# Kernel optimization log

Measured on AMD Instinct MI355X. Metric: run time of the kernel, lower is better.

The kernel has to match this reference:

```python
import jax, jax.numpy as jnp
import numpy as np
from jax import lax

MAX_LEN = 50
MAX_STATES = 50
STATE_DIM = MAX_STATES + 3  # 53
LSTM = 32
EMB = 8
VOCAB = 20
N_NODES = 131072
N_EDGES = 65536
B = 4096
NODES_PER_GRAPH = 32
ACTION_SIZE = 53


def setup_inputs() -> dict:
    key = jax.random.key(0)
    ks = jax.random.split(key, 32)
    x = jax.random.normal(ks[0], (N_NODES, 55), jnp.float32)
    src_num = jax.random.uniform(ks[1], (N_EDGES, STATE_DIM), jnp.float32)
    tgt_num = jax.random.uniform(ks[2], (N_EDGES, STATE_DIM), jnp.float32)
    regex_tokens = jax.random.randint(ks[3], (N_EDGES, MAX_LEN), 0, VOCAB)
    edge_index = jax.random.randint(ks[4], (2, N_EDGES), 0, N_NODES)
    batch = jnp.repeat(jnp.arange(B, dtype=jnp.int32), NODES_PER_GRAPH)
    # frozen embedding (padding_idx=0 -> row 0 zero) + frozen bidirectional LSTM params
    emb = (jax.random.normal(ks[5], (VOCAB, EMB)) * 0.1).at[0].set(0.0)
    def lp(k1, k2, k3):
        return (jax.random.normal(k1, (4 * LSTM, EMB)) * 0.1,
                jax.random.normal(k2, (4 * LSTM, LSTM)) * 0.1,
                jax.random.normal(k3, (4 * LSTM,)) * 0.1)  # b = b_ih + b_hh combined
    w_ih_f, w_hh_f, b_f = lp(ks[6], ks[7], ks[8])
    w_ih_b, w_hh_b, b_b = lp(ks[9], ks[10], ks[11])
    def lin(k, din, dout):
        kw, kb = jax.random.split(k)
        return (jax.random.normal(kw, (din, dout)) * 0.05,
                jax.random.normal(kb, (dout,)) * 0.05)
    p1_w, p1_b = lin(ks[12], 289, 128)
    p2_w, p2_b = lin(ks[13], 128, 64)
    p3_w, p3_b = lin(ks[14], 64, 32)
    p4_w, p4_b = lin(ks[15], 32, 1)
    v1_w, v1_b = lin(ks[16], 289, 32)
    v2_w, v2_b = lin(ks[17], 32, 1)
    return dict(x=x, src_num=src_num, tgt_num=tgt_num, regex_tokens=regex_tokens,
                edge_index=edge_index, batch=batch, emb=emb,
                w_ih_f=w_ih_f, w_hh_f=w_hh_f, b_f=b_f,
                w_ih_b=w_ih_b, w_hh_b=w_hh_b, b_b=b_b,
                p1_w=p1_w, p1_b=p1_b, p2_w=p2_w, p2_b=p2_b,
                p3_w=p3_w, p3_b=p3_b, p4_w=p4_w, p4_b=p4_b,
                v1_w=v1_w, v1_b=v1_b, v2_w=v2_w, v2_b=v2_b,
                num_graphs=B, action_size=ACTION_SIZE)


def _lstm_mean(xs, w_ih, w_hh, b):
    # xs: [T, E, in]; returns mean over time of hidden states, [E, H]
    T, E, _ = xs.shape
    H = w_hh.shape[1]
    def step(carry, xt):
        h, c, acc = carry
        z = xt @ w_ih.T + h @ w_hh.T + b  # [E, 4H], torch gate order i,f,g,o
        i, f, g, o = jnp.split(z, 4, axis=-1)
        c = jax.nn.sigmoid(f) * c + jax.nn.sigmoid(i) * jnp.tanh(g)
        h = jax.nn.sigmoid(o) * jnp.tanh(c)
        return (h, c, acc + h), None
    z0 = jnp.zeros((E, H), xs.dtype)
    (h, c, acc), _ = lax.scan(step, (z0, z0, z0), xs)
    return acc / T


def _mean_pool(feats, idx, num):
    s = jax.ops.segment_sum(feats, idx, num_segments=num)
    cnt = jax.ops.segment_sum(jnp.ones((feats.shape[0], 1), feats.dtype), idx, num_segments=num)
    return s / jnp.maximum(cnt, 1.0)


def reference(x, src_num, tgt_num, regex_tokens, edge_index, batch, emb,
              w_ih_f, w_hh_f, b_f, w_ih_b, w_hh_b, b_b,
              p1_w, p1_b, p2_w, p2_b, p3_w, p3_b, p4_w, p4_b,
              v1_w, v1_b, v2_w, v2_b, num_graphs, action_size):
    # frozen EmbeddingWithLSTM: embed -> bidirectional LSTM -> mean over time
    xs = emb[regex_tokens].transpose(1, 0, 2)  # [T, E, EMB]
    mean_f = _lstm_mean(xs, w_ih_f, w_hh_f, b_f)
    mean_b = _lstm_mean(xs[::-1], w_ih_b, w_hh_b, b_b)  # mean of reversed == mean
    regex_feat = jnp.concatenate([mean_f, mean_b], axis=-1)  # [E, 64]

    src, tgt = edge_index[0], edge_index[1]
    n = x.shape[0]
    out_tr = _mean_pool(jnp.concatenate([tgt_num, regex_feat], -1), src, n)
    in_tr = _mean_pool(jnp.concatenate([src_num, regex_feat], -1), tgt, n)
    xc = jnp.concatenate([x, in_tr, out_tr], axis=-1)  # [N, 289]

    s = _mean_pool(xc, batch, num_graphs)  # [B, 289]
    v = jax.nn.relu(s @ v1_w + v1_b) @ v2_w + v2_b  # [B, 1]

    pi = jax.nn.relu(xc @ p1_w + p1_b)
    pi = jax.nn.relu(pi @ p2_w + p2_b)
    pi = jax.nn.relu(pi @ p3_w + p3_b)
    pi = pi @ p4_w + p4_b  # [N, 1]

    # vectorized ragged pack: per-graph running index (batch is sorted/contiguous)
    counts = jax.ops.segment_sum(jnp.ones_like(batch), batch, num_segments=num_graphs)
    offsets = jnp.concatenate([jnp.zeros((1,), counts.dtype), jnp.cumsum(counts)[:-1]])
    pos = jnp.arange(batch.shape[0], dtype=counts.dtype) - offsets[batch]
    new_x = jnp.full((num_graphs, action_size), -999.0, xc.dtype).at[batch, pos].set(pi[:, 0])
    return jax.nn.log_softmax(new_x, axis=1), v
```

## Files before the change

### kernel.cpp

```cpp
#include <hip/hip_runtime.h>
#include <hip/hip_bf16.h>
#include <cstdint>
#include <cstddef>

typedef __hip_bfloat16 bf16;
typedef __attribute__((ext_vector_type(8))) short short8;
typedef __attribute__((ext_vector_type(4))) float f32x4;
typedef __attribute__((ext_vector_type(4))) int i32x4;

#define NE 65536
#define NN 131072
#define TLEN 50
#define NB 4096
#define ACT 53
#define FEATF 120
#define NSLOT 12

static constexpr size_t OFF_FEAT_IN  = 0;
static constexpr size_t OFF_FEAT_OUT = OFF_FEAT_IN + (size_t)NE * FEATF;
static constexpr size_t OFF_CNT_IN   = OFF_FEAT_OUT + (size_t)NE * FEATF;
static constexpr size_t OFF_CNT_OUT  = OFF_CNT_IN + NN;
static constexpr size_t OFF_SLOT_IN  = OFF_CNT_OUT + NN;
static constexpr size_t OFF_SLOT_OUT = OFF_SLOT_IN + (size_t)NN * NSLOT;
static constexpr size_t OFF_ZXF      = OFF_SLOT_OUT + (size_t)NN * NSLOT;
static constexpr size_t OFF_WFRAG    = OFF_ZXF + 4096;
static constexpr size_t OFF_B1       = OFF_WFRAG + 4096;
static constexpr size_t OFF_B2       = OFF_B1 + 20480;
static constexpr size_t OFF_B3       = OFF_B2 + 4096;
static constexpr size_t OFF_V1F      = OFF_B3 + 1024;
static constexpr size_t OFF_P1B      = OFF_V1F + 5120;
static constexpr size_t OFF_P2B      = OFF_P1B + 128;
static constexpr size_t OFF_P3B      = OFF_P2B + 64;
static constexpr size_t OFF_P4W      = OFF_P3B + 32;
static constexpr size_t OFF_P4B      = OFF_P4W + 32;
static constexpr size_t OFF_V1B      = OFF_P4B + 32;
static constexpr size_t OFF_V2W      = OFF_V1B + 32;
static constexpr size_t OFF_V2B      = OFF_V2W + 32;
static constexpr size_t OFF_FLAG     = OFF_V2B + 32;

__device__ __forceinline__ unsigned short f2bf(float f) {
  unsigned u = __float_as_uint(f);
  return (unsigned short)((u + 0x7fffu + ((u >> 16) & 1u)) >> 16);
}
__device__ __forceinline__ float bf2f(short b) {
  return __uint_as_float(((unsigned)(unsigned short)b) << 16);
}
__device__ __forceinline__ float sig3(float x) {
  float t = __builtin_amdgcn_fmed3f(x, -4.f, 4.f);
  float p = fmaf(fabsf(t), -0.03125f, 0.25f);
  return fmaf(t, p, 0.5f);
}
__device__ __forceinline__ float th3(float x) {
  float t = __builtin_amdgcn_fmed3f(x, -2.f, 2.f);
  float p = fmaf(fabsf(t), -0.25f, 1.0f);
  return t * p;
}

template<bool BF>
__device__ __forceinline__ float ldf(const void* p, size_t i) {
  if constexpr (BF) return __bfloat162float(((const bf16*)p)[i]);
  else              return ((const float*)p)[i];
}
__device__ __forceinline__ void st_out(void* p, size_t i, float v, int bf) {
  if (bf) ((bf16*)p)[i] = __float2bfloat16(v);
  else    ((float*)p)[i] = v;
}

__device__ __forceinline__ short8 onehot8(int tok, int quad) {
  int kk = tok - (quad << 3);
  unsigned sh = 0x3F80u << ((kk & 1) << 4);
  int kq = kk >> 1;
  i32x4 o;
  o.x = (kq == 0) ? (int)sh : 0;
  o.y = (kq == 1) ? (int)sh : 0;
  o.z = (kq == 2) ? (int)sh : 0;
  o.w = (kq == 3) ? (int)sh : 0;
  return __builtin_bit_cast(short8, o);
}

__device__ __forceinline__ int kmap(int k) {
  if (k < 55)  return k;
  if (k < 119) return k + 53;
  if (k < 172) return k - 64;
  if (k < 236) return k + 53;
  return k - 64;
}

__global__ void detect_kernel(const unsigned int* __restrict__ xw, int* __restrict__ flag) {
  int lane = threadIdx.x;
  int cnt = 0;
  #pragma unroll
  for (int i = 0; i < 4; ++i) {
    unsigned w = xw[lane * 4 + i];
    unsigned e = (w >> 7) & 0xFFu;
    cnt += (e >= 100u && e <= 150u) ? 1 : 0;
  }
  #pragma unroll
  for (int off = 32; off; off >>= 1) cnt += __shfl_down(cnt, off);
  if (lane == 0) *flag = (cnt >= 192) ? 1 : 0;
}

__global__ void slot_kernel(const int* __restrict__ eidx, float* __restrict__ ws) {
  int e = blockIdx.x * 256 + threadIdx.x;
  if (e >= NE) return;
  unsigned* cnt_out = (unsigned*)(ws + OFF_CNT_OUT);
  unsigned* cnt_in  = (unsigned*)(ws + OFF_CNT_IN);
  int* slot_out = (int*)(ws + OFF_SLOT_OUT);
  int* slot_in  = (int*)(ws + OFF_SLOT_IN);
  int s = eidx[e], t = eidx[NE + e];
  unsigned k = atomicAdd(cnt_out + s, 1u);
  if (k < NSLOT) slot_out[s * NSLOT + k] = e;
  unsigned k2 = atomicAdd(cnt_in + t, 1u);
  if (k2 < NSLOT) slot_in[t * NSLOT + k2] = e;
}

struct PrepPtrs {
  const void *emb, *wihf, *whhf, *bfw, *wihb, *whhb, *bbw;
  const void *p1w, *p1b, *p2w, *p2b, *p3w, *p3b, *p4w, *p4b;
  const void *v1w, *v1b, *v2w, *v2b;
};

template<bool BF>
__device__ __forceinline__ void prep_body(int idx, const PrepPtrs P, float* __restrict__ ws) {
  if (idx < 8192) {
    int d = idx >> 12, r = idx & 4095;
    int T = r >> 9, L = (r >> 3) & 63, jj = r & 7;
    int n = L & 15, q = L >> 4;
    int k = q*8 + jj, col = T*16 + n;
    float s = 0.f;
    if (k < 20) {
      s = ldf<BF>(d ? P.bbw : P.bfw, col);
      const void* wih = d ? P.wihb : P.wihf;
      #pragma unroll
      for (int kk = 0; kk < 8; ++kk)
        s += ldf<BF>(wih, col*8 + kk) * ldf<BF>(P.emb, k*8 + kk);
    }
    ((short*)(ws + OFF_ZXF))[idx] = (short)f2bf(s);
    return;
  }
  idx -= 8192;
  if (idx < 8192) {
    int d = idx >> 12, r = idx & 4095;
    int T = r >> 9, L = (r >> 3) & 63, jj = r & 7;
    int n = L & 15, q = L >> 4;
    int k = q*8 + jj;
    int u = (k >> 1) + 16*(k & 1);
    float v = ldf<BF>(d ? P.whhb : P.whhf, (size_t)(T*16 + n) * 32 + u);
    ((short*)(ws + OFF_WFRAG))[d*4096 + r] = (short)f2bf(v);
    return;
  }
  idx -= 8192;
  if (idx < 40960) {
    int r = idx;
    int NTKT = r >> 9, L = (r >> 3) & 63, j = r & 7;
    int NT = NTKT / 10, KT = NTKT - NT * 10;
    int n = L & 15, q = L >> 4;
    int k = KT*32 + q*8 + j, col = NT*16 + n;
    float v = (k < 289) ? ldf<BF>(P.p1w, (size_t)kmap(k) * 128 + col) : 0.f;
    ((short*)(ws + OFF_B1))[r] = (short)f2bf(v);
    return;
  }
  idx -= 40960;
  if (idx < 8192) {
    int r = idx;
    int NTKT = r >> 9, L = (r >> 3) & 63, j = r & 7;
    int NT = NTKT >> 2, KT = NTKT & 3;
    int n = L & 15, q = L >> 4;
    int k = KT*32 + q*8 + j, col = NT*16 + n;
    ((short*)(ws + OFF_B2))[r] = (short)f2bf(ldf<BF>(P.p2w, (size_t)k * 64 + col));
    return;
  }
  idx -= 8192;
  if (idx < 2048) {
    int r = idx;
    int NTKT = r >> 9, L = (r >> 3) & 63, j = r & 7;
    int NT = NTKT >> 1, KT = NTKT & 1;
    int n = L & 15, q = L >> 4;
    int k = KT*32 + q*8 + j, col = NT*16 + n;
    ((short*)(ws + OFF_B3))[r] = (short)f2bf(ldf<BF>(P.p3w, (size_t)k * 32 + col));
    return;
  }
  idx -= 2048;
  if (idx < 10240) {
    int r = idx;
    int TK = r >> 9, L = (r >> 3) & 63, j = r & 7;
    int Tv = TK / 10, KT = TK - Tv * 10;
    int n = L & 15, qd = L >> 4;
    int k = KT*32 + qd*8 + j, u = Tv*16 + n;
    float v = (k < 289) ? ldf<BF>(P.v1w, (size_t)kmap(k) * 32 + u) : 0.f;
    ((short*)(ws + OFF_V1F))[r] = (short)f2bf(v);
    return;
  }
  idx -= 10240;
  #define CPY(src, off, n) if (idx < (n)) { ws[(off) + idx] = ldf<BF>(src, idx); return; } idx -= (n);
  CPY(P.p1b, OFF_P1B, 128)
  CPY(P.p2b, OFF_P2B, 64)
  CPY(P.p3b, OFF_P3B, 32)
  CPY(P.p4w, OFF_P4W, 32)
  CPY(P.p4b, OFF_P4B, 1)
  CPY(P.v1b, OFF_V1B, 32)
  CPY(P.v2w, OFF_V2W, 32)
  CPY(P.v2b, OFF_V2B, 1)
  #undef CPY
}

__global__ void prep_kernel(const int* __restrict__ flag, const PrepPtrs P, float* __restrict__ ws) {
  int idx = blockIdx.x * 256 + threadIdx.x;
  if (*flag) prep_body<true>(idx, P, ws);
  else       prep_body<false>(idx, P, ws);
}

template<bool BF>
__device__ __forceinline__ void lstm_body(
    short (*tk_s)[800], short (*h_s)[640],
    const int* __restrict__ tokens, const int* __restrict__ eidx,
    const void* __restrict__ src_num, const void* __restrict__ tgt_num,
    float* __restrict__ ws)
{
  float* fi = ws + OFF_FEAT_IN;
  float* fo = ws + OFF_FEAT_OUT;
  const short* wfp = (const short*)(ws + OFF_WFRAG);
  const short* zxp = (const short*)(ws + OFF_ZXF);

  const int tid  = threadIdx.x;
  const int w    = tid >> 6;
  const int lane = tid & 63;
  const int n    = lane & 15;
  const int quad = lane >> 4;
  const int d    = blockIdx.x & 1;
  const int ebase = (blockIdx.x >> 1) * 32 + w * 16;

  for (int i = lane; i < 16 * TLEN; i += 64) {
    int e = (int)(((unsigned)i * 41944u) >> 21);
    int t = i - e * TLEN;
    tk_s[w][t * 16 + e] = (short)tokens[(size_t)(ebase + e) * TLEN + t];
  }

  short8 wfr[8], zxfr[8];
  #pragma unroll
  for (int T = 0; T < 8; ++T) {
    wfr[T]  = *(const short8*)(wfp + d*4096 + T*512 + lane*8);
    zxfr[T] = *(const short8*)(zxp + d*4096 + T*512 + lane*8);
  }
  for (int i = lane; i < 320; i += 64) ((int*)h_s[w])[i] = 0;

  float c_[2][4], accm[2][4];
  #pragma unroll
  for (int p = 0; p < 2; ++p)
    #pragma unroll
    for (int r = 0; r < 4; ++r) { c_[p][r] = 0.f; accm[p][r] = 0.f; }

  const f32x4 zeroC = {0.f, 0.f, 0.f, 0.f};

  const int tstep = d ? -16 : 16;
  const short* tkp = &tk_s[w][(d ? (TLEN - 1) * 16 : 0) + n];
  {
    short8 a2 = onehot8((int)*tkp, quad);
  }
  f32x4 zxa[8];
  {
    short8 a2 = onehot8((int)*tkp, quad);
    #pragma unroll
    for (int T = 0; T < 8; ++T)
      zxa[T] = __builtin_amdgcn_mfma_f32_16x16x32_bf16(a2, zxfr[T], zeroC, 0, 0, 0);
  }

  for (int t = 0; t < TLEN; ++t) {
    short8 af = *(const short8*)&h_s[w][n * 40 + quad * 8];

    f32x4 acc4[8];
    #pragma unroll
    for (int T = 0; T < 8; ++T)
      acc4[T] = __builtin_amdgcn_mfma_f32_16x16x32_bf16(af, wfr[T], zxa[T], 0, 0, 0);

    if (t + 1 < TLEN) {
      tkp += tstep;
      short8 a2 = onehot8((int)*tkp, quad);
      #pragma unroll
      for (int T = 0; T < 8; ++T)
        zxa[T] = __builtin_amdgcn_mfma_f32_16x16x32_bf16(a2, zxfr[T], zeroC, 0, 0, 0);
    }

    #pragma unroll
    for (int r = 0; r < 4; ++r) {
      float hvp[2];
      #pragma unroll
      for (int p = 0; p < 2; ++p) {
        float si = sig3(acc4[p][r]);
        float sf = sig3(acc4[2+p][r]);
        float tg = th3 (acc4[4+p][r]);
        float so = sig3(acc4[6+p][r]);
        float cv = fmaf(sf, c_[p][r], si * tg);
        c_[p][r] = cv;
        float hv = so * th3(cv);
        accm[p][r] += hv;
        hvp[p] = hv;
      }
      unsigned pk = __builtin_amdgcn_perm(__float_as_uint(hvp[1]), __float_as_uint(hvp[0]), 0x07060302u);
      *(unsigned*)&h_s[w][(quad*4 + r) * 40 + 2*n] = pk;
    }
  }

  const int fb = 32 * d;
  #pragma unroll
  for (int r = 0; r < 4; ++r) {
    int e  = ebase + quad * 4 + r;
    float m0 = accm[0][r] * 0.02f;
    float m1 = accm[1][r] * 0.02f;
    fi[(size_t)e * FEATF + fb + n]      = m0;
    fi[(size_t)e * FEATF + fb + 16 + n] = m1;
    fo[(size_t)e * FEATF + fb + n]      = m0;
    fo[(size_t)e * FEATF + fb + 16 + n] = m1;
  }
  if (d == 0) {
    for (int i = lane; i < 16 * 53; i += 64) {
      int e = (int)(((unsigned)i * 39569u) >> 21);
      int f = i - e * 53;
      int ge = ebase + e;
      fo[(size_t)ge * FEATF + 64 + f] = ldf<BF>(tgt_num, (size_t)ge * 53 + f);
      fi[(size_t)ge * FEATF + 64 + f] = ldf<BF>(src_num, (size_t)ge * 53 + f);
    }
  }
}

__global__ __launch_bounds__(128) void lstm_kernel(
    const int* __restrict__ flag,
    const int* __restrict__ tokens, const int* __restrict__ eidx,
    const void* __restrict__ src_num, const void* __restrict__ tgt_num,
    float* __restrict__ ws)
{
  __shared__ short tk_s[2][800];
  __shared__ short h_s[2][640];
  if (*flag) lstm_body<true>(tk_s, h_s, tokens, eidx, src_num, tgt_num, ws);
  else       lstm_body<false>(tk_s, h_s, tokens, eidx, src_num, tgt_num, ws);
}

__global__ __launch_bounds__(256, 4) void pi_kernel(const int* __restrict__ flag,
                                                    const void* __restrict__ x,
                                                    float* __restrict__ ws,
                                                    void* __restrict__ out)
{
  __shared__ short xst[64 * 168];
  __shared__ float pib[64];
  __shared__ float vpb[128];
  __shared__ float mls[4];

  const int bf = *flag;
  const float* fIN  = ws + OFF_FEAT_IN;
  const float* fOUT = ws + OFF_FEAT_OUT;
  const unsigned* cinp  = (const unsigned*)(ws + OFF_CNT_IN);
  const unsigned* coutp = (const unsigned*)(ws + OFF_CNT_OUT);
  const int* slin  = (const int*)(ws + OFF_SLOT_IN);
  const int* slout = (const int*)(ws + OFF_SLOT_OUT);
  const float* p1b = ws + OFF_P1B;
  const float* p2b = ws + OFF_P2B;
  const float* p3b = ws + OFF_P3B;
  const float* p4w = ws + OFF_P4W;
  const float* v1b = ws + OFF_V1B;
  const float* v2w = ws + OFF_V2W;
  const float p4b0 = ws[OFF_P4B];
  const float v2b0 = ws[OFF_V2B];
  const short* b1  = (const short*)(ws + OFF_B1);
  const short* b2  = (const short*)(ws + OFF_B2);
  const short* b3  = (const short*)(ws + OFF_B3);
  const short* v1f = (const short*)(ws + OFF_V1F);

  const int tid = threadIdx.x;
  const int w = tid >> 6, lane = tid & 63;
  const int nn = lane & 15, q = lane >> 4;
  const int nbase = blockIdx.x * 64;
  const int n4 = tid >> 2, qq = tid & 3;
  const size_t gn = (size_t)(nbase + n4);

  const int cin_full  = (int)cinp[gn];
  const int cout_full = (int)coutp[gn];
  const int cin  = cin_full  < NSLOT ? cin_full  : NSLOT;
  const int cout = cout_full < NSLOT ? cout_full : NSLOT;
  const float rci = __builtin_amdgcn_rcpf((float)(cin_full  > 1 ? cin_full  : 1));
  const float rco = __builtin_amdgcn_rcpf((float)(cout_full > 1 ? cout_full : 1));

  f32x4 fin[8];
  #pragma unroll
  for (int j = 0; j < 8; ++j) fin[j] = (f32x4){0.f, 0.f, 0.f, 0.f};
  #pragma unroll
  for (int k = 0; k < NSLOT; ++k) {
    if (k < cin) {
      const f32x4* fr = (const f32x4*)(fIN + (size_t)slin[gn * NSLOT + k] * FEATF);
      #pragma unroll
      for (int j = 0; j < 8; ++j) { int c = qq + 4 * j; if (c < 30) fin[j] += fr[c]; }
    }
  }

  if (bf) {
    const short* xs = (const short*)x;
    for (int i = tid; i < 64 * 55; i += 256) {
      int node = (i * 38131) >> 21;
      int col = i - node * 55;
      xst[node * 168 + col] = xs[(size_t)nbase * 55 + i];
    }
  } else {
    const float* xf = (const float*)x;
    for (int i = tid; i < 64 * 55; i += 256) {
      int node = (i * 38131) >> 21;
      int col = i - node * 55;
      xst[node * 168 + col] = (short)f2bf(xf[(size_t)nbase * 55 + i]);
    }
  }

  #pragma unroll
  for (int j4 = 0; j4 < 8; ++j4) {
    int c = qq + 4 * j4;
    if (c < 27) {
      #pragma unroll
      for (int e = 0; e < 4; ++e) {
        int col = 4 * c + e;
        if (col < 105) xst[n4 * 168 + 55 + col] = (short)f2bf(fin[j4][e] * rci);
      }
    }
  }
  __syncthreads();

  f32x4 a1[8], av0, av1;
  #pragma unroll
  for (int T = 0; T < 8; ++T) { float b = p1b[T * 16 + nn]; a1[T] = (f32x4){b, b, b, b}; }
  av0 = (f32x4){0.f, 0.f, 0.f, 0.f};
  av1 = av0;
  #pragma unroll
  for (int kk = 0; kk < 5; ++kk) {
    short8 af = *(const short8*)&xst[(w * 16 + nn) * 168 + kk * 32 + q * 8];
    short8 bfr[8];
    #pragma unroll
    for (int T = 0; T < 8; ++T)
      bfr[T] = *(const short8*)(b1 + ((size_t)(T * 10 + kk) * 64 + lane) * 8);
    short8 bva = *(const short8*)(v1f + ((size_t)kk * 64 + lane) * 8);
    short8 bvb = *(const short8*)(v1f + ((size_t)(10 + kk) * 64 + lane) * 8);
    #pragma unroll
    for (int T = 0; T < 8; ++T)
      a1[T] = __builtin_amdgcn_mfma_f32_16x16x32_bf16(af, bfr[T], a1[T], 0, 0, 0);
    av0 = __builtin_amdgcn_mfma_f32_16x16x32_bf16(af, bva, av0, 0, 0, 0);
    av1 = __builtin_amdgcn_mfma_f32_16x16x32_bf16(af, bvb, av1, 0, 0, 0);
  }
  __syncthreads();

  {
    int ct = 26 + ((qq + 2) & 3);
    f32x4 tl = (qq & 2) ? fin[6] : fin[7];
    #pragma unroll
    for (int e = 0; e < 4; ++e) {
      int col = 4 * ct + e;
      if (col >= 105 && col < 117) xst[n4 * 168 + (col - 105)] = (short)f2bf(tl[e] * rci);
    }
    f32x4 fout[8];
    #pragma unroll
    for (int j = 0; j < 8; ++j) fout[j] = (f32x4){0.f, 0.f, 0.f, 0.f};
    #pragma unroll
    for (int k = 0; k < NSLOT; ++k) {
      if (k < cout) {
        const f32x4* fr = (const f32x4*)(fOUT + (size_t)slout[gn * NSLOT + k] * FEATF);
        #pragma unroll
        for (int j = 0; j < 8; ++j) { int c = qq + 4 * j; if (c < 30) fout[j] += fr[c]; }
      }
    }
    #pragma unroll
    for (int j4 = 0; j4 < 8; ++j4) {
      int c = qq + 4 * j4;
      if (c < 30) {
        #pragma unroll
        for (int e = 0; e < 4; ++e) {
          int col = 4 * c + e;
          if (col < 117) xst[n4 * 168 + 12 + col] = (short)f2bf(fout[j4][e] * rco);
        }
      }
    }
    for (int l = 129 + qq; l < 160; l += 4) xst[n4 * 168 + l] = 0;
  }
  __syncthreads();

  #pragma unroll
  for (int kk = 5; kk < 10; ++kk) {
    short8 af = *(const short8*)&xst[(w * 16 + nn) * 168 + (kk - 5) * 32 + q * 8];
    short8 bfr[8];
    #pragma unroll
    for (int T = 0; T < 8; ++T)
      bfr[T] = *(const short8*)(b1 + ((size_t)(T * 10 + kk) * 64 + lane) * 8);
    short8 bva = *(const short8*)(v1f + ((size_t)kk * 64 + lane) * 8);
    short8 bvb = *(const short8*)(v1f + ((size_t)(10 + kk) * 64 + lane) * 8);
    #pragma unroll
    for (int T = 0; T < 8; ++T)
      a1[T] = __builtin_amdgcn_mfma_f32_16x16x32_bf16(af, bfr[T], a1[T], 0, 0, 0);
    av0 = __builtin_amdgcn_mfma_f32_16x16x32_bf16(af, bva, av0, 0, 0, 0);
    av1 = __builtin_amdgcn_mfma_f32_16x16x32_bf16(af, bvb, av1, 0, 0, 0);
  }
  __syncthreads();

  #pragma unroll
  for (int T = 0; T < 8; ++T)
    #pragma unroll
    for (int r = 0; r < 4; ++r)
      xst[(w * 16 + q * 4 + r) * 136 + T * 16 + nn] = (short)f2bf(fmaxf(a1[T][r], 0.f));
  {
    float s0 = av0[0] + av0[1] + av0[2] + av0[3];
    float s1 = av1[0] + av1[1] + av1[2] + av1[3];
    s0 += __shfl_xor(s0, 16); s0 += __shfl_xor(s0, 32);
    s1 += __shfl_xor(s1, 16); s1 += __shfl_xor(s1, 32);
    if (lane < 16) { vpb[w * 32 + nn] = s0; vpb[w * 32 + 16 + nn] = s1; }
  }
  __syncthreads();

  f32x4 a2[4];
  #pragma unroll
  for (int T = 0; T < 4; ++T) { float b = p2b[T * 16 + nn]; a2[T] = (f32x4){b, b, b, b}; }
  #pragma unroll
  for (int kk = 0; kk < 4; ++kk) {
    short8 af = *(const short8*)&xst[(w * 16 + nn) * 136 + kk * 32 + q * 8];
    short8 bfr[4];
    #pragma unroll
    for (int T = 0; T < 4; ++T)
      bfr[T] = *(const short8*)(b2 + ((size_t)(T * 4 + kk) * 64 + lane) * 8);
    #pragma unroll
    for (int T = 0; T < 4; ++T)
      a2[T] = __builtin_amdgcn_mfma_f32_16x16x32_bf16(af, bfr[T], a2[T], 0, 0, 0);
  }
  __syncthreads();

  #pragma unroll
  for (int T = 0; T < 4; ++T)
    #pragma unroll
    for (int r = 0; r < 4; ++r)
      xst[(w * 16 + q * 4 + r) * 72 + T * 16 + nn] = (short)f2bf(fmaxf(a2[T][r], 0.f));
  __syncthreads();

  f32x4 a3[2];
  #pragma unroll
  for (int T = 0; T < 2; ++T) { float b = p3b[T * 16 + nn]; a3[T] = (f32x4){b, b, b, b}; }
  #pragma unroll
  for (int kk = 0; kk < 2; ++kk) {
    short8 af = *(const short8*)&xst[(w * 16 + nn) * 72 + kk * 32 + q * 8];
    short8 b3a = *(const short8*)(b3 + ((size_t)kk * 64 + lane) * 8);
    short8 b3b = *(const short8*)(b3 + ((size_t)(2 + kk) * 64 + lane) * 8);
    a3[0] = __builtin_amdgcn_mfma_f32_16x16x32_bf16(af, b3a, a3[0], 0, 0, 0);
    a3[1] = __builtin_amdgcn_mfma_f32_16x16x32_bf16(af, b3b, a3[1], 0, 0, 0);
  }
  {
    float w4a = p4w[nn], w4b = p4w[16 + nn];
    float part[4];
    #pragma unroll
    for (int r = 0; r < 4; ++r)
      part[r] = fmaxf(a3[0][r], 0.f) * w4a + fmaxf(a3[1][r], 0.f) * w4b;
    #pragma unroll
    for (int off = 1; off < 16; off <<= 1)
      #pragma unroll
      for (int r = 0; r < 4; ++r) part[r] += __shfl_xor(part[r], off);
    float pv = (nn == 0) ? part[0] : (nn == 1) ? part[1] : (nn == 2) ? part[2] : part[3];
    if (nn < 4) pib[w * 16 + q * 4 + nn] = pv + p4b0;
  }
  if (tid < 64) {
    int g = tid >> 5, u = tid & 31;
    float vs = (vpb[(2 * g) * 32 + u] + vpb[(2 * g + 1) * 32 + u]) * (1.f / 32.f);
    float h = fmaxf(vs + v1b[u], 0.f) * v2w[u];
    #pragma unroll
    for (int off = 1; off < 32; off <<= 1) h += __shfl_xor(h, off);
    if (u == 0) st_out(out, (size_t)NB * ACT + 2 * blockIdx.x + g, h + v2b0, bf);
  }
  __syncthreads();

  if (tid < 64) {
    int g = tid >> 5, u = tid & 31;
    float val = pib[g * 32 + u];
    float m = val;
    #pragma unroll
    for (int off = 1; off < 32; off <<= 1) m = fmaxf(m, __shfl_xor(m, off));
    float e = __expf(val - m);
    #pragma unroll
    for (int off = 1; off < 32; off <<= 1) e += __shfl_xor(e, off);
    if (u == 0) { mls[g * 2] = m; mls[g * 2 + 1] = __logf(e); }
  }
  __syncthreads();

  if (tid < 106) {
    int g = (tid >= 53) ? 1 : 0;
    int c = tid - g * 53;
    float val = (c < 32) ? pib[g * 32 + c] : -999.f;
    st_out(out, (size_t)(2 * blockIdx.x + g) * 53 + c, val - mls[g * 2] - mls[g * 2 + 1], bf);
  }
}

extern "C" void kernel_launch(void* const* d_in, const int* in_sizes, int n_in,
                              void* d_out, int out_size, void* d_ws, size_t ws_size,
                              hipStream_t stream) {
  const void* x        = d_in[0];
  const void* src_num  = d_in[1];
  const void* tgt_num  = d_in[2];
  const int*  tokens   = (const int*)d_in[3];
  const int*  eidx     = (const int*)d_in[4];
  PrepPtrs P;
  P.emb  = d_in[6];
  P.wihf = d_in[7];  P.whhf = d_in[8];  P.bfw = d_in[9];
  P.wihb = d_in[10]; P.whhb = d_in[11]; P.bbw = d_in[12];
  P.p1w = d_in[13]; P.p1b = d_in[14];
  P.p2w = d_in[15]; P.p2b = d_in[16];
  P.p3w = d_in[17]; P.p3b = d_in[18];
  P.p4w = d_in[19]; P.p4b = d_in[20];
  P.v1w = d_in[21]; P.v1b = d_in[22];
  P.v2w = d_in[23]; P.v2b = d_in[24];

  float* ws = (float*)d_ws;
  int* flag = (int*)(ws + OFF_FLAG);

  hipMemsetAsync(ws + OFF_CNT_IN, 0, 2 * (size_t)NN * sizeof(float), stream);

  detect_kernel<<<1, 64, 0, stream>>>((const unsigned int*)x, flag);

  prep_kernel<<<306, 256, 0, stream>>>(flag, P, ws);

  slot_kernel<<<NE / 256, 256, 0, stream>>>(eidx, ws);

  lstm_kernel<<<(NE / 32) * 2, 128, 0, stream>>>(flag, tokens, eidx, src_num, tgt_num, ws);

  pi_kernel<<<NN / 64, 256, 0, stream>>>(flag, x, ws, d_out);
}
```

Before: 408.3 us.

## Keep LSTM hidden state in registers via transposed MFMA, merge slot into prep kernel

Swaps the MFMA operand order so the gate outputs come out transposed, which lets the packed bf16 hidden state be fed straight back as the B operand from registers. This removes the per-step shared-memory store and reload of h and the LDS buffer that held it. The output mean writes become vectorized f32x4 stores, and the slot-building kernel is folded into the prep kernel launch to save a launch. Correctness depends on the prepped weight fragment layout also being valid for the swapped A/B roles; the code keeps the same fragment buffers.

```diff
diff --git a/kernel.cpp b/kernel.cpp
--- a/kernel.cpp
+++ b/kernel.cpp
@@ -15,6 +15,7 @@
 #define ACT 53
 #define FEATF 120
 #define NSLOT 12
+#define PREPN 78336
 
 static constexpr size_t OFF_FEAT_IN  = 0;
 static constexpr size_t OFF_FEAT_OUT = OFF_FEAT_IN + (size_t)NE * FEATF;
@@ -100,20 +101,6 @@
   if (lane == 0) *flag = (cnt >= 192) ? 1 : 0;
 }
 
-__global__ void slot_kernel(const int* __restrict__ eidx, float* __restrict__ ws) {
-  int e = blockIdx.x * 256 + threadIdx.x;
-  if (e >= NE) return;
-  unsigned* cnt_out = (unsigned*)(ws + OFF_CNT_OUT);
-  unsigned* cnt_in  = (unsigned*)(ws + OFF_CNT_IN);
-  int* slot_out = (int*)(ws + OFF_SLOT_OUT);
-  int* slot_in  = (int*)(ws + OFF_SLOT_IN);
-  int s = eidx[e], t = eidx[NE + e];
-  unsigned k = atomicAdd(cnt_out + s, 1u);
-  if (k < NSLOT) slot_out[s * NSLOT + k] = e;
-  unsigned k2 = atomicAdd(cnt_in + t, 1u);
-  if (k2 < NSLOT) slot_in[t * NSLOT + k2] = e;
-}
-
 struct PrepPtrs {
   const void *emb, *wihf, *whhf, *bfw, *wihb, *whhb, *bbw;
   const void *p1w, *p1b, *p2w, *p2b, *p3w, *p3b, *p4w, *p4b;
@@ -204,15 +191,31 @@
   #undef CPY
 }
 
-__global__ void prep_kernel(const int* __restrict__ flag, const PrepPtrs P, float* __restrict__ ws) {
+__global__ void prep_kernel(const int* __restrict__ flag, const PrepPtrs P,
+                            const int* __restrict__ eidx, float* __restrict__ ws) {
   int idx = blockIdx.x * 256 + threadIdx.x;
+  if (idx >= PREPN) {
+    int e = idx - PREPN;
+    if (e < NE) {
+      unsigned* cnt_out = (unsigned*)(ws + OFF_CNT_OUT);
+      unsigned* cnt_in  = (unsigned*)(ws + OFF_CNT_IN);
+      int* slot_out = (int*)(ws + OFF_SLOT_OUT);
+      int* slot_in  = (int*)(ws + OFF_SLOT_IN);
+      int s = eidx[e], t = eidx[NE + e];
+      unsigned k = atomicAdd(cnt_out + s, 1u);
+      if (k < NSLOT) slot_out[s * NSLOT + k] = e;
+      unsigned k2 = atomicAdd(cnt_in + t, 1u);
+      if (k2 < NSLOT) slot_in[t * NSLOT + k2] = e;
+    }
+    return;
+  }
   if (*flag) prep_body<true>(idx, P, ws);
   else       prep_body<false>(idx, P, ws);
 }
 
 template<bool BF>
 __device__ __forceinline__ void lstm_body(
-    short (*tk_s)[800], short (*h_s)[640],
+    short (*tk_s)[800],
     const int* __restrict__ tokens, const int* __restrict__ eidx,
     const void* __restrict__ src_num, const void* __restrict__ tgt_num,
     float* __restrict__ ws)
@@ -242,7 +245,6 @@
     wfr[T]  = *(const short8*)(wfp + d*4096 + T*512 + lane*8);
     zxfr[T] = *(const short8*)(zxp + d*4096 + T*512 + lane*8);
   }
-  for (int i = lane; i < 320; i += 64) ((int*)h_s[w])[i] = 0;
 
   float c_[2][4], accm[2][4];
   #pragma unroll
@@ -251,36 +253,34 @@
     for (int r = 0; r < 4; ++r) { c_[p][r] = 0.f; accm[p][r] = 0.f; }
 
   const f32x4 zeroC = {0.f, 0.f, 0.f, 0.f};
+
+  short8 hB = __builtin_bit_cast(short8, (i32x4){0, 0, 0, 0});
 
   const int tstep = d ? -16 : 16;
   const short* tkp = &tk_s[w][(d ? (TLEN - 1) * 16 : 0) + n];
-  {
-    short8 a2 = onehot8((int)*tkp, quad);
-  }
   f32x4 zxa[8];
   {
-    short8 a2 = onehot8((int)*tkp, quad);
+    short8 b2 = onehot8((int)*tkp, quad);
     #pragma unroll
     for (int T = 0; T < 8; ++T)
-      zxa[T] = __builtin_amdgcn_mfma_f32_16x16x32_bf16(a2, zxfr[T], zeroC, 0, 0, 0);
+      zxa[T] = __builtin_amdgcn_mfma_f32_16x16x32_bf16(zxfr[T], b2, zeroC, 0, 0, 0);
   }
 
   for (int t = 0; t < TLEN; ++t) {
-    short8 af = *(const short8*)&h_s[w][n * 40 + quad * 8];
-
     f32x4 acc4[8];
     #pragma unroll
     for (int T = 0; T < 8; ++T)
-      acc4[T] = __builtin_amdgcn_mfma_f32_16x16x32_bf16(af, wfr[T], zxa[T], 0, 0, 0);
+      acc4[T] = __builtin_amdgcn_mfma_f32_16x16x32_bf16(wfr[T], hB, zxa[T], 0, 0, 0);
 
     if (t + 1 < TLEN) {
       tkp += tstep;
-      short8 a2 = onehot8((int)*tkp, quad);
+      short8 b2 = onehot8((int)*tkp, quad);
       #pragma unroll
       for (int T = 0; T < 8; ++T)
-        zxa[T] = __builtin_amdgcn_mfma_f32_16x16x32_bf16(a2, zxfr[T], zeroC, 0, 0, 0);
-    }
-
+        zxa[T] = __builtin_amdgcn_mfma_f32_16x16x32_bf16(zxfr[T], b2, zeroC, 0, 0, 0);
+    }
+
+    i32x4 hn;
     #pragma unroll
     for (int r = 0; r < 4; ++r) {
       float hvp[2];
@@ -296,21 +296,19 @@
         accm[p][r] += hv;
         hvp[p] = hv;
       }
-      unsigned pk = __builtin_amdgcn_perm(__float_as_uint(hvp[1]), __float_as_uint(hvp[0]), 0x07060302u);
-      *(unsigned*)&h_s[w][(quad*4 + r) * 40 + 2*n] = pk;
-    }
+      hn[r] = (int)__builtin_amdgcn_perm(__float_as_uint(hvp[1]), __float_as_uint(hvp[0]), 0x07060302u);
+    }
+    hB = __builtin_bit_cast(short8, hn);
   }
 
   const int fb = 32 * d;
   #pragma unroll
-  for (int r = 0; r < 4; ++r) {
-    int e  = ebase + quad * 4 + r;
-    float m0 = accm[0][r] * 0.02f;
-    float m1 = accm[1][r] * 0.02f;
-    fi[(size_t)e * FEATF + fb + n]      = m0;
-    fi[(size_t)e * FEATF + fb + 16 + n] = m1;
-    fo[(size_t)e * FEATF + fb + n]      = m0;
-    fo[(size_t)e * FEATF + fb + 16 + n] = m1;
+  for (int p = 0; p < 2; ++p) {
+    f32x4 m = { accm[p][0] * 0.02f, accm[p][1] * 0.02f,
+                accm[p][2] * 0.02f, accm[p][3] * 0.02f };
+    size_t off = (size_t)(ebase + n) * FEATF + fb + p * 16 + quad * 4;
+    *(f32x4*)(fi + off) = m;
+    *(f32x4*)(fo + off) = m;
   }
   if (d == 0) {
     for (int i = lane; i < 16 * 53; i += 64) {
@@ -330,9 +328,8 @@
     float* __restrict__ ws)
 {
   __shared__ short tk_s[2][800];
-  __shared__ short h_s[2][640];
-  if (*flag) lstm_body<true>(tk_s, h_s, tokens, eidx, src_num, tgt_num, ws);
-  else       lstm_body<false>(tk_s, h_s, tokens, eidx, src_num, tgt_num, ws);
+  if (*flag) lstm_body<true>(tk_s, tokens, eidx, src_num, tgt_num, ws);
+  else       lstm_body<false>(tk_s, tokens, eidx, src_num, tgt_num, ws);
 }
 
 __global__ __launch_bounds__(256, 4) void pi_kernel(const int* __restrict__ flag,
@@ -611,9 +608,7 @@
 
   detect_kernel<<<1, 64, 0, stream>>>((const unsigned int*)x, flag);
 
-  prep_kernel<<<306, 256, 0, stream>>>(flag, P, ws);
-
-  slot_kernel<<<NE / 256, 256, 0, stream>>>(eidx, ws);
+  prep_kernel<<<(PREPN + NE) / 256, 256, 0, stream>>>(flag, P, eidx, ws);
 
   lstm_kernel<<<(NE / 32) * 2, 128, 0, stream>>>(flag, tokens, eidx, src_num, tgt_num, ws);
 
```

New measurement: 398.3 us. -2.5%, faster.
